# Kernel optimization log

Measured on AMD Instinct MI355X. Metric: run time of the kernel, lower is better.

Reference implementation:

```python
import jax, jax.numpy as jnp
import numpy as np

B, L, C, H, V = 64, 512, 256, 4, 32000
D = C // H
DIL = (1, 2, 4)
WIN = 3
NC = (50, 20)
NEG = -1e9


def setup_inputs() -> dict:
    key = jax.random.key(0)
    ks = jax.random.split(key, 20)
    g = lambda i, shape: jax.random.normal(ks[i], shape, jnp.float32) * 0.05
    Lay = len(DIL)
    x = jax.random.randint(ks[0], (B, L), 0, V)
    emb = g(1, (V, C)).at[0].set(0.0)  # padding_idx=0 row is zero
    return dict(
        x=x, emb=emb, pos=g(2, (L, C)),
        gp_W=g(3, (Lay, C, C)), gp_as=g(4, (Lay, H, D)), gp_ad=g(5, (Lay, H, D)),
        gf_W=g(6, (Lay, C, C)), gf_as=g(7, (Lay, H, D)), gf_ad=g(8, (Lay, H, D)),
        msg_W=g(9, (Lay, C, 2 * C)), msg_b=jnp.zeros((Lay, C), jnp.float32),
        gru_Wih=g(10, (Lay, 3 * C, C)), gru_bih=jnp.zeros((Lay, 3 * C), jnp.float32),
        gru_Whh=g(11, (Lay, 3 * C, C)), gru_bhh=jnp.zeros((Lay, 3 * C), jnp.float32),
        ln_g=jnp.ones((Lay, C), jnp.float32), ln_b=jnp.zeros((Lay, C), jnp.float32),
        pool_w=g(12, (C,)), pool_b=jnp.zeros((), jnp.float32),
        h0_W=g(13, (NC[0], C)), h0_b=jnp.zeros((NC[0],), jnp.float32),
        h1_W=g(14, (NC[1], C)), h1_b=jnp.zeros((NC[1],), jnp.float32),
    )


def _dense_gat(x, W, a_src, a_dst, adj):
    # x: [B,L,C], W: [C_out,C_in], a_*: [H,D], adj: [B,L,L] bool
    b, l, _ = x.shape
    h = jnp.einsum('blc,oc->blo', x, W).reshape(b, l, H, D).transpose(0, 2, 1, 3)  # [B,H,L,D]
    s = jnp.einsum('bhld,hd->bhl', h, a_src)
    d = jnp.einsum('bhld,hd->bhl', h, a_dst)
    e = s[:, :, :, None] + d[:, :, None, :]            # [B,H,L,L]
    e = jnp.where(e > 0, e, 0.2 * e)                   # LeakyReLU(0.2)
    e = jnp.where(adj[:, None, :, :], e, NEG)
    alpha = jax.nn.softmax(e, axis=-1)                 # dropout is identity in eval
    out = jnp.einsum('bhij,bhjd->bhid', alpha, h)
    return out.transpose(0, 2, 1, 3).reshape(b, l, C)


def _forward(x, emb, pos, gp_W, gp_as, gp_ad, gf_W, gf_as, gf_ad,
             msg_W, msg_b, gru_Wih, gru_bih, gru_Whh, gru_bhh,
             ln_g, ln_b, pool_w, pool_b, h0_W, h0_b, h1_W, h1_b):
    mask = x != 0                                      # [B,L]
    mf = mask.astype(jnp.float32)[..., None]           # [B,L,1]
    h = (emb[x] + pos[None, :, :] * mf) * mf
    logical = jnp.clip(jnp.cumsum(mask.astype(jnp.int32), axis=1) - 1, 0)
    valid = mask[:, None, :] & mask[:, :, None]        # [B,L,L]
    eye = jnp.eye(L, dtype=bool)[None]
    for l in range(len(DIL)):
        dil = DIL[l]
        diff = logical[:, :, None] - logical[:, None, :]
        ad = jnp.abs(diff)
        in_win = (ad <= WIN * dil) & (ad % dil == 0)
        adj_p = (valid & in_win & (diff < 0)) | eye
        adj_f = (valid & in_win & (diff > 0)) | eye
        m_p = _dense_gat(h, gp_W[l], gp_as[l], gp_ad[l], adj_p)
        m_f = _dense_gat(h, gf_W[l], gf_as[l], gf_ad[l], adj_f)
        m = jnp.concatenate([m_p, m_f], axis=-1)
        m = jax.nn.relu(jnp.einsum('blk,ck->blc', m, msg_W[l]) + msg_b[l])
        # GRUCell(input=m, hidden=h), PyTorch gate order: r,z,n
        gi = jnp.einsum('blc,gc->blg', m, gru_Wih[l]) + gru_bih[l]
        gh = jnp.einsum('blc,gc->blg', h, gru_Whh[l]) + gru_bhh[l]
        ir, iz, inn = jnp.split(gi, 3, axis=-1)
        hr, hz, hn = jnp.split(gh, 3, axis=-1)
        r = jax.nn.sigmoid(ir + hr)
        z = jax.nn.sigmoid(iz + hz)
        n = jnp.tanh(inn + r * hn)
        h_new = (1.0 - z) * n + z * h
        mu = jnp.mean(h_new, axis=-1, keepdims=True)
        var = jnp.mean(jnp.square(h_new - mu), axis=-1, keepdims=True)
        h_new = (h_new - mu) * jax.lax.rsqrt(var + 1e-5) * ln_g[l] + ln_b[l]
        h = h_new * mf
    # attention pooling over sequence (masked softmax on linear scores)
    sc = jnp.einsum('blc,c->bl', h, pool_w) + pool_b
    sc = jnp.where(mask, sc, NEG)
    a = jax.nn.softmax(sc, axis=-1)
    pooled = jnp.einsum('bl,blc->bc', a, h)            # dropout identity in eval
    o0 = pooled @ h0_W.T + h0_b
    o1 = pooled @ h1_W.T + h1_b
    return jnp.concatenate([o0, o1], axis=-1)          # [B, 50+20]


def reference(x, emb, pos, gp_W, gp_as, gp_ad, gf_W, gf_as, gf_ad,
              msg_W, msg_b, gru_Wih, gru_bih, gru_Whh, gru_bhh,
              ln_g, ln_b, pool_w, pool_b, h0_W, h0_b, h1_W, h1_b):
    return _forward(x, emb, pos, gp_W, gp_as, gp_ad, gf_W, gf_as, gf_ad,
                    msg_W, msg_b, gru_Wih, gru_bih, gru_Whh, gru_bhh,
                    ln_g, ln_b, pool_w, pool_b, h0_W, h0_b, h1_W, h1_b)
```

## Files before the change

### kernel.cpp

```cpp
#include <hip/hip_runtime.h>
#include <math.h>

#define B_ 64
#define L_ 512
#define C_ 256
#define H_ 4
#define LAY 3
#define NEGV -1e9f

#define GF_BIAS  1
#define GF_RELU  2
#define GF_OBF16 4

typedef __attribute__((ext_vector_type(8))) short short8;
typedef __attribute__((ext_vector_type(4))) short short4v;
typedef __attribute__((ext_vector_type(4))) float floatx4;

static __device__ __forceinline__ float rcp_(float x) { return __builtin_amdgcn_rcpf(x); }
static __device__ __forceinline__ float sig_(float x) { return rcp_(1.f + __expf(-x)); }
static __device__ __forceinline__ float tanh_(float x) {
    float e = __expf(2.f * x);
    return 1.f - 2.f * rcp_(e + 1.f);
}

static __device__ __forceinline__ short f2bf(float f) {
    unsigned x = __float_as_uint(f);
    x += 0x7fffu + ((x >> 16) & 1u);
    return (short)(x >> 16);
}
static __device__ __forceinline__ float bf2f(short s) {
    return __uint_as_float(((unsigned)(unsigned short)s) << 16);
}

static __device__ __forceinline__ int tok_swizzle(int blk) {
    int c8 = blk & 7, i = blk >> 3;
    return (c8 + 8 * (i >> 5)) * 128 + (i & 31) * 4;
}

static __device__ __forceinline__ void gl_lds16(const short* g, short* l) {
    __builtin_amdgcn_global_load_lds(
        (const __attribute__((address_space(1))) unsigned int*)g,
        (__attribute__((address_space(3))) unsigned int*)l, 16, 0, 0);
}

#define CF() asm volatile("" ::: "memory")

__global__ void scan_kernel(const int* __restrict__ x, int* __restrict__ mask,
                            int* __restrict__ logical, int* __restrict__ pol,
                            int* __restrict__ nvalid) {
    int b = blockIdx.x, t = threadIdx.x;
    __shared__ int s[L_];
    int m = (x[b * L_ + t] != 0) ? 1 : 0;
    s[t] = m;
    __syncthreads();
    for (int off = 1; off < L_; off <<= 1) {
        int v = (t >= off) ? s[t - off] : 0;
        __syncthreads();
        s[t] += v;
        __syncthreads();
    }
    int cum = s[t];
    int lg = cum - 1; if (lg < 0) lg = 0;
    mask[b * L_ + t] = m;
    logical[b * L_ + t] = lg;
    if (m) pol[b * L_ + lg] = t;
    if (t == L_ - 1) nvalid[b] = cum;
}

__global__ void embed_kernel(const int* __restrict__ x, const float* __restrict__ emb,
                             const float* __restrict__ pos, short* __restrict__ hb) {
    int t = threadIdx.x;
    int bl = tok_swizzle(blockIdx.x) + (t >> 6);
    int lane = t & 63;
    int xv = x[bl];
    float mf = (xv != 0) ? 1.f : 0.f;
    int l = bl & (L_ - 1);
    float4 e = *(const float4*)&emb[(size_t)xv * C_ + lane * 4];
    float4 p = *(const float4*)&pos[(size_t)l * C_ + lane * 4];
    short4v hv4;
    hv4.x = f2bf((e.x + p.x * mf) * mf);
    hv4.y = f2bf((e.y + p.y * mf) * mf);
    hv4.z = f2bf((e.z + p.z * mf) * mf);
    hv4.w = f2bf((e.w + p.w * mf) * mf);
    *(short4v*)&hb[(size_t)bl * C_ + lane * 4] = hv4;
}

__global__ void f2bf_kernel(const float* __restrict__ s, short* __restrict__ d, int n) {
    int i = blockIdx.x * 256 + threadIdx.x;
    if (i < n) d[i] = f2bf(s[i]);
}

__global__ void prep_wcomb(const float* __restrict__ gpW, const float* __restrict__ gfW,
                           const float* __restrict__ gpas, const float* __restrict__ gpad,
                           const float* __restrict__ gfas, const float* __restrict__ gfad,
                           short* __restrict__ Wc) {
    int i = blockIdx.x * 256 + threadIdx.x;
    if (i >= 3 * 640 * 256) return;
    int k = i & 255;
    int r = (i >> 8) % 640;
    int l = i / (640 * 256);
    float v = 0.f;
    if (r < 256) {
        v = gpW[((size_t)l * 256 + r) * 256 + k];
    } else if (r < 512) {
        v = gfW[((size_t)l * 256 + (r - 256)) * 256 + k];
    } else {
        int n = r - 512;
        if (n < 16) {
            int type = n >> 3, dir = (n >> 2) & 1, hh = n & 3;
            const float* a = type ? (dir ? gfad : gpad) : (dir ? gfas : gpas);
            const float* W = dir ? gfW : gpW;
            for (int j = 0; j < 64; j++) {
                float av = a[l * 256 + hh * 64 + j];
                float wv = W[((size_t)l * 256 + hh * 64 + j) * 256 + k];
                v = fmaf(av, wv, v);
            }
        }
    }
    Wc[i] = f2bf(v);
}

__global__ void prep_gru_i(const float* __restrict__ Wih, const float* __restrict__ Whh,
                           short* __restrict__ Bc) {
    int i = blockIdx.x * 256 + threadIdx.x;
    if (i >= 3 * 1024 * 512) return;
    int k = i & 511, np = (i >> 9) & 1023, l = i >> 19;
    int ch = np >> 2, g = np & 3;
    float v = 0.f;
    if (g < 2) {
        v = (k < 256) ? Wih[((size_t)l * 768 + g * 256 + ch) * 256 + k]
                      : Whh[((size_t)l * 768 + g * 256 + ch) * 256 + (k - 256)];
    } else if (g == 2) {
        if (k < 256) v = Wih[((size_t)l * 768 + 512 + ch) * 256 + k];
    } else {
        if (k >= 256) v = Whh[((size_t)l * 768 + 512 + ch) * 256 + (k - 256)];
    }
    Bc[i] = f2bf(v);
}

__global__ void prep_bias4(const float* __restrict__ bih, const float* __restrict__ bhh,
                           float* __restrict__ bc) {
    int i = blockIdx.x * 256 + threadIdx.x;
    if (i >= 3 * 1024) return;
    int np = i & 1023, l = i >> 10;
    int ch = np >> 2, g = np & 3;
    float v;
    if (g < 2)       v = bih[l * 768 + g * 256 + ch] + bhh[l * 768 + g * 256 + ch];
    else if (g == 2) v = bih[l * 768 + 512 + ch];
    else             v = bhh[l * 768 + 512 + ch];
    bc[i] = v;
}

__global__ __launch_bounds__(256) void bgemm(const short* __restrict__ A0,
                                             const short* __restrict__ Bw,
                                             void* __restrict__ Cout,
                                             const float* __restrict__ bias,
                                             int K, int lda, int ldc, int nstore,
                                             int cbBits, int flags) {
    __shared__ short As[128 * 32];
    __shared__ short Bs[128 * 32];
    const int id = blockIdx.x;
    const int nrb8 = gridDim.x >> (3 + cbBits);
    const int j = id >> 3;
    const int cb = j / nrb8;
    const int rb = (id & 7) * nrb8 + (j % nrb8);
    const int tid = threadIdx.x;
    const int wave = tid >> 6, lane = tid & 63;
    const int wm = wave >> 1, wn = wave & 1;
    const size_t arow0 = (size_t)rb * 128;
    const short* Bb = Bw + (size_t)cb * 128 * K;
    floatx4 acc[4][4];
#pragma unroll
    for (int i = 0; i < 4; i++)
#pragma unroll
        for (int jj = 0; jj < 4; jj++) acc[i][jj] = (floatx4)0.f;

    const int srow = lane >> 2;
    const int sq = (lane & 3) * 8;
    const int q = lane >> 4, t16 = lane & 15;

    for (int k0 = 0; k0 < K; k0 += 32) {
        const short* Abase = A0 + arow0 * (size_t)lda + k0;
#pragma unroll
        for (int t = 0; t < 2; ++t) {
            int r = (wave * 2 + t) * 16 + srow;
            gl_lds16(Abase + (size_t)r * lda + sq, &As[r * 32 + sq]);
            gl_lds16(Bb + (size_t)r * K + k0 + sq, &Bs[r * 32 + sq]);
        }
        __syncthreads();
        short8 af[4], bfr[4];
#pragma unroll
        for (int mf = 0; mf < 4; mf++)
            af[mf] = *(const short8*)&As[(wm * 64 + mf * 16 + t16) * 32 + q * 8];
#pragma unroll
        for (int nf = 0; nf < 4; nf++)
            bfr[nf] = *(const short8*)&Bs[(wn * 64 + nf * 16 + t16) * 32 + q * 8];
#pragma unroll
        for (int mf = 0; mf < 4; mf++)
#pragma unroll
            for (int nf = 0; nf < 4; nf++)
                acc[nf][mf] = __builtin_amdgcn_mfma_f32_16x16x32_bf16(
                    bfr[nf], af[mf], acc[nf][mf], 0, 0, 0);
        __syncthreads();
    }

    const int rowbase = rb * 128 + wm * 64;
    const int colbase = cb * 128 + wn * 64;
#pragma unroll
    for (int nf = 0; nf < 4; nf++) {
        int col0 = colbase + nf * 16 + q * 4;
        if (col0 >= nstore) continue;
        float4 bv4 = make_float4(0.f, 0.f, 0.f, 0.f);
        if (flags & GF_BIAS) bv4 = *(const float4*)&bias[col0];
#pragma unroll
        for (int mf = 0; mf < 4; mf++) {
            int row = rowbase + mf * 16 + t16;
            float v0 = acc[nf][mf][0] + bv4.x;
            float v1 = acc[nf][mf][1] + bv4.y;
            float v2 = acc[nf][mf][2] + bv4.z;
            float v3 = acc[nf][mf][3] + bv4.w;
            if (flags & GF_RELU) {
                v0 = fmaxf(v0, 0.f); v1 = fmaxf(v1, 0.f);
                v2 = fmaxf(v2, 0.f); v3 = fmaxf(v3, 0.f);
            }
            size_t base = (size_t)row * ldc + col0;
            if (flags & GF_OBF16) {
                short4v pk;
                pk.x = f2bf(v0); pk.y = f2bf(v1); pk.z = f2bf(v2); pk.w = f2bf(v3);
                *(short4v*)&((short*)Cout)[base] = pk;
            } else {
                float4 pk = make_float4(v0, v1, v2, v3);
                *(float4*)&((float*)Cout)[base] = pk;
            }
        }
    }
}

__global__ __launch_bounds__(256) void projssd_bgemm(const short* __restrict__ A0,
                                                     const short* __restrict__ Bw,
                                                     short* __restrict__ hpb2,
                                                     float* __restrict__ Ssd) {
    __shared__ short As[128 * 32];
    __shared__ short Bs[128 * 32];
    const int id = blockIdx.x;
    const int j = id >> 3;
    const int cb = j >> 5;
    const int rb = ((id & 7) << 5) + (j & 31);
    const int tid = threadIdx.x;
    const int wave = tid >> 6, lane = tid & 63;
    const int wm = wave >> 1, wn = wave & 1;
    const size_t arow0 = (size_t)rb * 128;
    const short* Bb = Bw + (size_t)cb * 128 * 256;
    floatx4 acc[4][4];
#pragma unroll
    for (int i = 0; i < 4; i++)
#pragma unroll
        for (int jj = 0; jj < 4; jj++) acc[i][jj] = (floatx4)0.f;

    const int srow = lane >> 2;
    const int sq = (lane & 3) * 8;
    const int q = lane >> 4, t16 = lane & 15;

    for (int k0 = 0; k0 < 256; k0 += 32) {
        const short* Abase = A0 + arow0 * 256 + k0;
#pragma unroll
        for (int t = 0; t < 2; ++t) {
            int r = (wave * 2 + t) * 16 + srow;
            gl_lds16(Abase + (size_t)r * 256 + sq, &As[r * 32 + sq]);
            gl_lds16(Bb + (size_t)r * 256 + k0 + sq, &Bs[r * 32 + sq]);
        }
        __syncthreads();
        short8 af[4], bfr[4];
#pragma unroll
        for (int mf = 0; mf < 4; mf++)
            af[mf] = *(const short8*)&As[(wm * 64 + mf * 16 + t16) * 32 + q * 8];
#pragma unroll
        for (int nf = 0; nf < 4; nf++)
            bfr[nf] = *(const short8*)&Bs[(wn * 64 + nf * 16 + t16) * 32 + q * 8];
#pragma unroll
        for (int mf = 0; mf < 4; mf++)
#pragma unroll
            for (int nf = 0; nf < 4; nf++)
                acc[nf][mf] = __builtin_amdgcn_mfma_f32_16x16x32_bf16(
                    bfr[nf], af[mf], acc[nf][mf], 0, 0, 0);
        __syncthreads();
    }

    const int rowbase = rb * 128 + wm * 64;
    if (cb < 4) {
        const int colbase = cb * 128 + wn * 64;
#pragma unroll
        for (int nf = 0; nf < 4; nf++) {
            int col0 = colbase + nf * 16 + q * 4;
#pragma unroll
            for (int mf = 0; mf < 4; mf++) {
                int row = rowbase + mf * 16 + t16;
                short4v pk;
                pk.x = f2bf(acc[nf][mf][0]);
                pk.y = f2bf(acc[nf][mf][1]);
                pk.z = f2bf(acc[nf][mf][2]);
                pk.w = f2bf(acc[nf][mf][3]);
                *(short4v*)&hpb2[(size_t)row * 512 + col0] = pk;
            }
        }
    } else {
        if (wn == 0) {
            int col0 = q * 4;
            if (col0 < 16) {
#pragma unroll
                for (int mf = 0; mf < 4; mf++) {
                    int row = rowbase + mf * 16 + t16;
                    float4 pk = make_float4(acc[0][mf][0], acc[0][mf][1],
                                            acc[0][mf][2], acc[0][mf][3]);
                    *(float4*)&Ssd[(size_t)row * 16 + col0] = pk;
                }
            }
        }
    }
}

static __device__ __forceinline__ short8 lds_rd8(const short* p) {
    return *(const short8*)p;
}

template <int MH>
static __device__ __forceinline__ void ld_af(const short* bufA, int wm, int q, int t16,
                                             short8 af[4][2]) {
#pragma unroll
    for (int mfl = 0; mfl < 4; ++mfl) {
        int row = wm * 128 + (MH * 4 + mfl) * 16 + t16;
#pragma unroll
        for (int ks = 0; ks < 2; ++ks) {
            int cg = (ks * 4 + q) ^ (row & 7);
            af[mfl][ks] = lds_rd8(&bufA[row * 64 + cg * 8]);
        }
    }
}

template <int NH>
static __device__ __forceinline__ void ld_bf(const short* bufB, int wn, int q, int t16,
                                             short8 bf[2][2]) {
#pragma unroll
    for (int nfl = 0; nfl < 2; ++nfl) {
        int row = wn * 64 + (NH * 2 + nfl) * 16 + t16;
#pragma unroll
        for (int ks = 0; ks < 2; ++ks) {
            int cg = (ks * 4 + q) ^ (row & 7);
            bf[nfl][ks] = lds_rd8(&bufB[row * 64 + cg * 8]);
        }
    }
}

template <int MH, int NH>
static __device__ __forceinline__ void mfma_q(const short8 af[4][2], const short8 bf[2][2],
                                              floatx4 acc[4][8]) {
    __builtin_amdgcn_s_setprio(1);
#pragma unroll
    for (int ks = 0; ks < 2; ++ks)
#pragma unroll
        for (int mfl = 0; mfl < 4; ++mfl)
#pragma unroll
            for (int nfl = 0; nfl < 2; ++nfl)
                acc[NH * 2 + nfl][MH * 4 + mfl] = __builtin_amdgcn_mfma_f32_16x16x32_bf16(
                    bf[nfl][ks], af[mfl][ks], acc[NH * 2 + nfl][MH * 4 + mfl], 0, 0, 0);
    __builtin_amdgcn_s_setprio(0);
}

__global__ __launch_bounds__(512, 2) void gru_bgemm(const short* __restrict__ mmb,
                                                    const short* __restrict__ hb_in,
                                                    const short* __restrict__ Bw,
                                                    short* __restrict__ hn2b,
                                                    const float* __restrict__ bias4) {
    __shared__ short lds[2][32768];
    const int id = blockIdx.x;
    const int rb = 16 * (id & 7) + (id >> 5);
    const int cb = (id >> 3) & 3;
    const int tid = threadIdx.x;
    const int wave = tid >> 6, lane = tid & 63;
    const int wm = wave >> 2, wn = wave & 3;
    const int q = lane >> 4, t16 = lane & 15;
    const size_t arow0 = (size_t)rb * 256;
    const short* Bb = Bw + (size_t)cb * 256 * 512;
    const int ord0 = (5 + cb) & 7;

    floatx4 acc[4][8];
#pragma unroll
    for (int i = 0; i < 4; i++)
#pragma unroll
        for (int jj = 0; jj < 8; jj++) acc[i][jj] = (floatx4)0.f;

    auto stageA = [&](int i, int Hh) {
        int tt = (ord0 + i) & 7;
        const short* Asrc = (tt < 4) ? (mmb + tt * 64) : (hb_in + (tt - 4) * 64);
        short* bufA = lds[i & 1];
#pragma unroll
        for (int u = 0; u < 2; ++u) {
            int unit = u * 512 + tid;
            int row = Hh * 128 + (unit >> 3);
            int cs = (unit & 7) ^ (row & 7);
            gl_lds16(Asrc + (arow0 + (size_t)row) * 256 + cs * 8,
                     bufA + Hh * 8192 + unit * 8);
        }
    };
    auto stageB = [&](int i, int Hh) {
        int tt = (ord0 + i) & 7;
        short* bufB = lds[i & 1] + 16384;
#pragma unroll
        for (int u = 0; u < 2; ++u) {
            int unit = u * 512 + tid;
            int row = Hh * 128 + (unit >> 3);
            int cs = (unit & 7) ^ (row & 7);
            gl_lds16(Bb + (size_t)row * 512 + tt * 64 + cs * 8,
                     bufB + Hh * 8192 + unit * 8);
        }
    };

    stageA(0, 0); stageA(0, 1); stageB(0, 0); stageB(0, 1);
    stageA(1, 0); stageA(1, 1); stageB(1, 0); stageB(1, 1);
    asm volatile("s_waitcnt vmcnt(8)" ::: "memory");
    CF(); __builtin_amdgcn_s_barrier(); CF();

    short8 af[4][2], b0[2][2], b1[2][2];

#pragma unroll
    for (int t = 0; t < 8; ++t) {
        const short* bufA = lds[t & 1];
        const short* bufB = lds[t & 1] + 16384;

        ld_af<0>(bufA, wm, q, t16, af);
        ld_bf<0>(bufB, wn, q, t16, b0);
        CF(); __builtin_amdgcn_s_barrier();
        asm volatile("s_waitcnt lgkmcnt(0)" ::: "memory");
        __builtin_amdgcn_sched_barrier(0);
        mfma_q<0, 0>(af, b0, acc);
        CF(); __builtin_amdgcn_s_barrier(); CF();

        ld_bf<1>(bufB, wn, q, t16, b1);
        CF(); __builtin_amdgcn_s_barrier();
        asm volatile("s_waitcnt lgkmcnt(0)" ::: "memory");
        __builtin_amdgcn_sched_barrier(0);
        mfma_q<0, 1>(af, b1, acc);
        CF(); __builtin_amdgcn_s_barrier(); CF();

        ld_af<1>(bufA, wm, q, t16, af);
        if (t < 6) { stageB(t + 2, 0); stageB(t + 2, 1); }
        CF(); __builtin_amdgcn_s_barrier();
        asm volatile("s_waitcnt lgkmcnt(0)" ::: "memory");
        __builtin_amdgcn_sched_barrier(0);
        mfma_q<1, 1>(af, b1, acc);
        CF(); __builtin_amdgcn_s_barrier(); CF();

        if (t < 6) { stageA(t + 2, 0); stageA(t + 2, 1); }
        CF(); __builtin_amdgcn_s_barrier();
        mfma_q<1, 0>(af, b0, acc);
        if (t < 6)       asm volatile("s_waitcnt vmcnt(8)" ::: "memory");
        else if (t == 6) asm volatile("s_waitcnt vmcnt(0)" ::: "memory");
        CF(); __builtin_amdgcn_s_barrier(); CF();
    }

    const short* hpt = lds[1];
    short* sO = (short*)lds;
#pragma unroll
    for (int nf = 0; nf < 4; nf++) {
        int chl = wn * 16 + nf * 4 + q;
        int col0 = cb * 256 + wn * 64 + nf * 16 + q * 4;
        float4 bv4 = *(const float4*)&bias4[col0];
#pragma unroll
        for (int mf = 0; mf < 8; mf++) {
            int rowl = wm * 128 + mf * 16 + t16;
            float hp = bf2f(hpt[rowl * 64 + (((chl >> 3) ^ (rowl & 7)) << 3) + (chl & 7)]);
            float r = sig_(acc[nf][mf][0] + bv4.x);
            float z = sig_(acc[nf][mf][1] + bv4.y);
            float nv = tanh_((acc[nf][mf][2] + bv4.z) + r * (acc[nf][mf][3] + bv4.w));
            sO[rowl * 72 + chl] = f2bf((1.f - z) * nv + z * hp);
        }
    }
    __syncthreads();
#pragma unroll
    for (int it = 0; it < 4; ++it) {
        int unit = it * 512 + tid;
        int rowl = unit >> 3, ck = unit & 7;
        *(short8*)&hn2b[(arow0 + rowl) * 256 + cb * 64 + ck * 8] =
            *(const short8*)&sO[rowl * 72 + ck * 8];
    }
}

__global__ __launch_bounds__(256) void ln_kernel(
    const short* __restrict__ hn2b, short* __restrict__ hb,
    const int* __restrict__ mask,
    const float* __restrict__ lng, const float* __restrict__ lnb) {
    int t = threadIdx.x;
    int bl = tok_swizzle(blockIdx.x) + (t >> 6);
    int lane = t & 63;
    short4v v4 = *(const short4v*)&hn2b[(size_t)bl * C_ + lane * 4];
    float v[4] = {bf2f(v4.x), bf2f(v4.y), bf2f(v4.z), bf2f(v4.w)};
    float s = (v[0] + v[1]) + (v[2] + v[3]);
    float ss = (v[0] * v[0] + v[1] * v[1]) + (v[2] * v[2] + v[3] * v[3]);
#pragma unroll
    for (int off = 32; off; off >>= 1) {
        s += __shfl_xor(s, off);
        ss += __shfl_xor(ss, off);
    }
    float mu = s * (1.f / 256.f);
    float var = ss * (1.f / 256.f) - mu * mu;
    float rstd = rsqrtf(fmaxf(var, 0.f) + 1e-5f);
    float4 lg = *(const float4*)&lng[lane * 4];
    float4 lb = *(const float4*)&lnb[lane * 4];
    float mfv = mask[bl] ? 1.f : 0.f;
    short4v yb;
    yb.x = f2bf(((v[0] - mu) * rstd * lg.x + lb.x) * mfv);
    yb.y = f2bf(((v[1] - mu) * rstd * lg.y + lb.y) * mfv);
    yb.z = f2bf(((v[2] - mu) * rstd * lg.z + lb.z) * mfv);
    yb.w = f2bf(((v[3] - mu) * rstd * lg.w + lb.w) * mfv);
    *(short4v*)&hb[(size_t)bl * C_ + lane * 4] = yb;
}

__global__ __launch_bounds__(256) void agg_fused(
    const short* __restrict__ hpb2, const float* __restrict__ S,
    const int* __restrict__ mask, const int* __restrict__ logical,
    const int* __restrict__ pol, const int* __restrict__ nvalid,
    short* __restrict__ m, int dil) {
    int t = threadIdx.x;
    int bl = tok_swizzle(blockIdx.x) + (t >> 6);
    int sub = t & 63;
    int dir = sub >> 5;
    int slot = sub & 31;
    int cb = slot * 8;
    int head = slot >> 3;
    int b = bl >> 9;

    int mi = mask[bl];
    int li = logical[bl];
    int nv = nvalid[b];
    int js[3]; int nn = 0;
    if (mi) {
#pragma unroll
        for (int k = 1; k <= 3; k++) {
            int lj = dir ? (li - k * dil) : (li + k * dil);
            if (lj >= 0 && lj < nv) js[nn++] = pol[b * L_ + lj];
        }
    }
    int sn = dir * 4 + head, dn = 8 + sn;
    float si = S[(size_t)bl * 16 + sn];
    float di = S[(size_t)bl * 16 + dn];
    float e0 = si + di; e0 = e0 > 0.f ? e0 : 0.2f * e0;
    float emax = e0, ev[3];
    for (int k = 0; k < nn; k++) {
        float djv = S[((size_t)(b * L_ + js[k])) * 16 + dn];
        float e = si + djv; e = e > 0.f ? e : 0.2f * e;
        ev[k] = e; emax = fmaxf(emax, e);
    }
    float w0 = __expf(e0 - emax), den = w0;
    float wv[3];
    for (int k = 0; k < nn; k++) { wv[k] = __expf(ev[k] - emax); den += wv[k]; }
    float rden = rcp_(den);

    size_t base = (size_t)bl * 512 + dir * 256 + cb;
    short8 vself = *(const short8*)&hpb2[base];
    float o[8];
#pragma unroll
    for (int j = 0; j < 8; j++) o[j] = w0 * bf2f(vself[j]);
    for (int k = 0; k < nn; k++) {
        short8 vn = *(const short8*)&hpb2[((size_t)(b * L_ + js[k])) * 512 + dir * 256 + cb];
#pragma unroll
        for (int j = 0; j < 8; j++) o[j] = fmaf(wv[k], bf2f(vn[j]), o[j]);
    }
    short8 ov;
#pragma unroll
    for (int j = 0; j < 8; j++) ov[j] = f2bf(o[j] * rden);
    *(short8*)&m[base] = ov;
}

__global__ __launch_bounds__(1024) void pool_head_kernel(
    const short* __restrict__ hb, const int* __restrict__ mask,
    const float* __restrict__ pw, const float* __restrict__ pb,
    const float* __restrict__ h0W, const float* __restrict__ h0b,
    const float* __restrict__ h1W, const float* __restrict__ h1b,
    float* __restrict__ out) {
    int b = blockIdx.x;
    int t = threadIdx.x;
    int lane = t & 63, wave = t >> 6;
    __shared__ float sc[L_];
    __shared__ float red[20];
    __shared__ float part[4][C_];
    __shared__ float pooled[C_];

    float4 wv = *(const float4*)&pw[lane * 4];
    for (int l = wave; l < L_; l += 16) {
        short4v hv = *(const short4v*)&hb[((size_t)b * L_ + l) * C_ + lane * 4];
        float p = bf2f(hv.x) * wv.x + bf2f(hv.y) * wv.y
                + bf2f(hv.z) * wv.z + bf2f(hv.w) * wv.w;
#pragma unroll
        for (int off = 32; off; off >>= 1) p += __shfl_down(p, off);
        if (lane == 0) sc[l] = mask[b * L_ + l] ? (p + pb[0]) : NEGV;
    }
    __syncthreads();

    float v = (t < L_) ? sc[t] : NEGV;
    float mx = v;
#pragma unroll
    for (int off = 32; off; off >>= 1) mx = fmaxf(mx, __shfl_down(mx, off));
    if (lane == 0) red[wave] = mx;
    __syncthreads();
    if (t == 0) {
        float g = red[0];
        for (int i = 1; i < 16; i++) g = fmaxf(g, red[i]);
        red[16] = g;
    }
    __syncthreads();
    float gmax = red[16];
    float e = (t < L_) ? __expf(v - gmax) : 0.f;
    float ssum = e;
#pragma unroll
    for (int off = 32; off; off >>= 1) ssum += __shfl_down(ssum, off);
    if (lane == 0) red[wave] = ssum;
    __syncthreads();
    if (t == 0) {
        float g = 0.f;
        for (int i = 0; i < 16; i++) g += red[i];
        red[17] = 1.f / g;
    }
    __syncthreads();
    if (t < L_) sc[t] = e * red[17];
    __syncthreads();

    int g = t >> 8, c = t & 255;
    const short* hrow = &hb[((size_t)b * L_ + g * 128) * C_ + c];
    const float* scg = &sc[g * 128];
    float a0 = 0.f, a1 = 0.f, a2 = 0.f, a3 = 0.f;
    for (int l = 0; l < 128; l += 4) {
        a0 = fmaf(scg[l + 0], bf2f(hrow[(size_t)(l + 0) * C_]), a0);
        a1 = fmaf(scg[l + 1], bf2f(hrow[(size_t)(l + 1) * C_]), a1);
        a2 = fmaf(scg[l + 2], bf2f(hrow[(size_t)(l + 2) * C_]), a2);
        a3 = fmaf(scg[l + 3], bf2f(hrow[(size_t)(l + 3) * C_]), a3);
    }
    part[g][c] = (a0 + a1) + (a2 + a3);
    __syncthreads();
    if (t < C_) pooled[t] = (part[0][t] + part[1][t]) + (part[2][t] + part[3][t]);
    __syncthreads();

    for (int o = wave; o < 70; o += 16) {
        const float* W = (o < 50) ? (h0W + (size_t)o * C_) : (h1W + (size_t)(o - 50) * C_);
        float bb = (o < 50) ? h0b[o] : h1b[o - 50];
        float4 w4 = *(const float4*)&W[lane * 4];
        float4 p4 = *(const float4*)&pooled[lane * 4];
        float s = p4.x * w4.x + p4.y * w4.y + p4.z * w4.z + p4.w * w4.w;
#pragma unroll
        for (int off = 32; off; off >>= 1) s += __shfl_down(s, off);
        if (lane == 0) out[b * 70 + o] = s + bb;
    }
}

extern "C" void kernel_launch(void* const* d_in, const int* in_sizes, int n_in,
                              void* d_out, int out_size, void* d_ws, size_t ws_size,
                              hipStream_t stream) {
    const int*   x    = (const int*)d_in[0];
    const float* emb  = (const float*)d_in[1];
    const float* pos  = (const float*)d_in[2];
    const float* gpW  = (const float*)d_in[3];
    const float* gpas = (const float*)d_in[4];
    const float* gpad = (const float*)d_in[5];
    const float* gfW  = (const float*)d_in[6];
    const float* gfas = (const float*)d_in[7];
    const float* gfad = (const float*)d_in[8];
    const float* msgW = (const float*)d_in[9];
    const float* msgb = (const float*)d_in[10];
    const float* Wih  = (const float*)d_in[11];
    const float* bih  = (const float*)d_in[12];
    const float* Whh  = (const float*)d_in[13];
    const float* bhh  = (const float*)d_in[14];
    const float* lng  = (const float*)d_in[15];
    const float* lnb  = (const float*)d_in[16];
    const float* pw   = (const float*)d_in[17];
    const float* pb   = (const float*)d_in[18];
    const float* h0W  = (const float*)d_in[19];
    const float* h0b  = (const float*)d_in[20];
    const float* h1W  = (const float*)d_in[21];
    const float* h1b  = (const float*)d_in[22];
    float* out = (float*)d_out;

    const size_t MW = 1024 * 1024;
    float* ws = (float*)d_ws;
    short* hn2b = (short*)ws;
    short* hb   = (short*)(ws + 8 * MW);
    short* mmb  = (short*)(ws + 12 * MW);
    float* Ssd  = ws + 12 * MW;
    short* hpb2 = (short*)(ws + 16 * MW);
    short* mb   = (short*)(ws + 24 * MW);
    short* Wcomb = (short*)(ws + 32 * MW);
    short* msgWb = Wcomb + 3 * 640 * 256;
    short* Bcat  = msgWb + 3 * 256 * 512;
    float* bias4 = (float*)(Bcat + 3 * 1024 * 512);
    int* mask    = (int*)(bias4 + 3 * 1024);
    int* logical = mask + B_ * L_;
    int* pol     = logical + B_ * L_;
    int* nvalid  = pol + B_ * L_;

    prep_wcomb<<<(3 * 640 * 256 + 255) / 256, 256, 0, stream>>>(gpW, gfW, gpas, gpad,
                                                                gfas, gfad, Wcomb);
    f2bf_kernel<<<(3 * 256 * 512 + 255) / 256, 256, 0, stream>>>(msgW, msgWb, 3 * 256 * 512);
    prep_gru_i<<<(3 * 1024 * 512 + 255) / 256, 256, 0, stream>>>(Wih, Whh, Bcat);
    prep_bias4<<<12, 256, 0, stream>>>(bih, bhh, bias4);

    scan_kernel<<<B_, L_, 0, stream>>>(x, mask, logical, pol, nvalid);
    embed_kernel<<<B_ * L_ / 4, 256, 0, stream>>>(x, emb, pos, hb);

    const int DILS[LAY] = {1, 2, 4};

    for (int l = 0; l < LAY; l++) {
        int dil = DILS[l];
        projssd_bgemm<<<256 * 5, 256, 0, stream>>>(hb, Wcomb + (size_t)l * 640 * 256,
                                                   hpb2, Ssd);
        agg_fused<<<8192, 256, 0, stream>>>(hpb2, Ssd, mask, logical, pol, nvalid, mb, dil);
        bgemm<<<256 * 2, 256, 0, stream>>>(mb, msgWb + (size_t)l * 256 * 512,
                                           mmb, msgb + l * C_, 512, 512, 256, 256, 1,
                                           GF_BIAS | GF_RELU | GF_OBF16);
        gru_bgemm<<<512, 512, 0, stream>>>(mmb, hb, Bcat + (size_t)l * 1024 * 512,
                                           hn2b, bias4 + l * 1024);
        ln_kernel<<<8192, 256, 0, stream>>>(hn2b, hb, mask, lng + l * C_, lnb + l * C_);
    }

    pool_head_kernel<<<B_, 1024, 0, stream>>>(hb, mask, pw, pb, h0W, h0b, h1W, h1b, out);
}
```

Measured before the change: 513.4 us.

## Replace generic message GEMM with pipelined 256x128-tile kernel; relax GRU scheduling

The generic 128x128 bgemm used for the message projection is replaced with a dedicated msg_bgemm. It uses 256x128 tiles, 512 threads and double-buffered swizzled LDS staging with async global-to-LDS loads that overlap the MFMA work. The epilogue applies bias and ReLU, converts to bf16, and writes coalesced output through LDS. Separately, the GRU GEMM loop drops its sched_barriers and goes from full unrolling to unroll 2, which gives the compiler more scheduling freedom but may change instruction interleaving.

```diff
diff --git a/kernel.cpp b/kernel.cpp
--- a/kernel.cpp
+++ b/kernel.cpp
@@ -7,10 +7,6 @@
 #define H_ 4
 #define LAY 3
 #define NEGV -1e9f
-
-#define GF_BIAS  1
-#define GF_RELU  2
-#define GF_OBF16 4
 
 typedef __attribute__((ext_vector_type(8))) short short8;
 typedef __attribute__((ext_vector_type(4))) short short4v;
@@ -151,91 +147,6 @@
     bc[i] = v;
 }
 
-__global__ __launch_bounds__(256) void bgemm(const short* __restrict__ A0,
-                                             const short* __restrict__ Bw,
-                                             void* __restrict__ Cout,
-                                             const float* __restrict__ bias,
-                                             int K, int lda, int ldc, int nstore,
-                                             int cbBits, int flags) {
-    __shared__ short As[128 * 32];
-    __shared__ short Bs[128 * 32];
-    const int id = blockIdx.x;
-    const int nrb8 = gridDim.x >> (3 + cbBits);
-    const int j = id >> 3;
-    const int cb = j / nrb8;
-    const int rb = (id & 7) * nrb8 + (j % nrb8);
-    const int tid = threadIdx.x;
-    const int wave = tid >> 6, lane = tid & 63;
-    const int wm = wave >> 1, wn = wave & 1;
-    const size_t arow0 = (size_t)rb * 128;
-    const short* Bb = Bw + (size_t)cb * 128 * K;
-    floatx4 acc[4][4];
-#pragma unroll
-    for (int i = 0; i < 4; i++)
-#pragma unroll
-        for (int jj = 0; jj < 4; jj++) acc[i][jj] = (floatx4)0.f;
-
-    const int srow = lane >> 2;
-    const int sq = (lane & 3) * 8;
-    const int q = lane >> 4, t16 = lane & 15;
-
-    for (int k0 = 0; k0 < K; k0 += 32) {
-        const short* Abase = A0 + arow0 * (size_t)lda + k0;
-#pragma unroll
-        for (int t = 0; t < 2; ++t) {
-            int r = (wave * 2 + t) * 16 + srow;
-            gl_lds16(Abase + (size_t)r * lda + sq, &As[r * 32 + sq]);
-            gl_lds16(Bb + (size_t)r * K + k0 + sq, &Bs[r * 32 + sq]);
-        }
-        __syncthreads();
-        short8 af[4], bfr[4];
-#pragma unroll
-        for (int mf = 0; mf < 4; mf++)
-            af[mf] = *(const short8*)&As[(wm * 64 + mf * 16 + t16) * 32 + q * 8];
-#pragma unroll
-        for (int nf = 0; nf < 4; nf++)
-            bfr[nf] = *(const short8*)&Bs[(wn * 64 + nf * 16 + t16) * 32 + q * 8];
-#pragma unroll
-        for (int mf = 0; mf < 4; mf++)
-#pragma unroll
-            for (int nf = 0; nf < 4; nf++)
-                acc[nf][mf] = __builtin_amdgcn_mfma_f32_16x16x32_bf16(
-                    bfr[nf], af[mf], acc[nf][mf], 0, 0, 0);
-        __syncthreads();
-    }
-
-    const int rowbase = rb * 128 + wm * 64;
-    const int colbase = cb * 128 + wn * 64;
-#pragma unroll
-    for (int nf = 0; nf < 4; nf++) {
-        int col0 = colbase + nf * 16 + q * 4;
-        if (col0 >= nstore) continue;
-        float4 bv4 = make_float4(0.f, 0.f, 0.f, 0.f);
-        if (flags & GF_BIAS) bv4 = *(const float4*)&bias[col0];
-#pragma unroll
-        for (int mf = 0; mf < 4; mf++) {
-            int row = rowbase + mf * 16 + t16;
-            float v0 = acc[nf][mf][0] + bv4.x;
-            float v1 = acc[nf][mf][1] + bv4.y;
-            float v2 = acc[nf][mf][2] + bv4.z;
-            float v3 = acc[nf][mf][3] + bv4.w;
-            if (flags & GF_RELU) {
-                v0 = fmaxf(v0, 0.f); v1 = fmaxf(v1, 0.f);
-                v2 = fmaxf(v2, 0.f); v3 = fmaxf(v3, 0.f);
-            }
-            size_t base = (size_t)row * ldc + col0;
-            if (flags & GF_OBF16) {
-                short4v pk;
-                pk.x = f2bf(v0); pk.y = f2bf(v1); pk.z = f2bf(v2); pk.w = f2bf(v3);
-                *(short4v*)&((short*)Cout)[base] = pk;
-            } else {
-                float4 pk = make_float4(v0, v1, v2, v3);
-                *(float4*)&((float*)Cout)[base] = pk;
-            }
-        }
-    }
-}
-
 __global__ __launch_bounds__(256) void projssd_bgemm(const short* __restrict__ A0,
                                                      const short* __restrict__ Bw,
                                                      short* __restrict__ hpb2,
@@ -351,6 +262,19 @@
     }
 }
 
+static __device__ __forceinline__ void ld_bf32(const short* bufB, int wn, int q, int t16,
+                                               short8 bf[2][2]) {
+#pragma unroll
+    for (int nfl = 0; nfl < 2; ++nfl) {
+        int row = wn * 32 + nfl * 16 + t16;
+#pragma unroll
+        for (int ks = 0; ks < 2; ++ks) {
+            int cg = (ks * 4 + q) ^ (row & 7);
+            bf[nfl][ks] = lds_rd8(&bufB[row * 64 + cg * 8]);
+        }
+    }
+}
+
 template <int MH, int NH>
 static __device__ __forceinline__ void mfma_q(const short8 af[4][2], const short8 bf[2][2],
                                               floatx4 acc[4][8]) {
@@ -363,6 +287,21 @@
             for (int nfl = 0; nfl < 2; ++nfl)
                 acc[NH * 2 + nfl][MH * 4 + mfl] = __builtin_amdgcn_mfma_f32_16x16x32_bf16(
                     bf[nfl][ks], af[mfl][ks], acc[NH * 2 + nfl][MH * 4 + mfl], 0, 0, 0);
+    __builtin_amdgcn_s_setprio(0);
+}
+
+template <int MH>
+static __device__ __forceinline__ void mfma_m(const short8 af[4][2], const short8 bf[2][2],
+                                              floatx4 acc[2][8]) {
+    __builtin_amdgcn_s_setprio(1);
+#pragma unroll
+    for (int ks = 0; ks < 2; ++ks)
+#pragma unroll
+        for (int mfl = 0; mfl < 4; ++mfl)
+#pragma unroll
+            for (int nfl = 0; nfl < 2; ++nfl)
+                acc[nfl][MH * 4 + mfl] = __builtin_amdgcn_mfma_f32_16x16x32_bf16(
+                    bf[nfl][ks], af[mfl][ks], acc[nfl][MH * 4 + mfl], 0, 0, 0);
     __builtin_amdgcn_s_setprio(0);
 }
 
@@ -422,7 +361,7 @@
 
     short8 af[4][2], b0[2][2], b1[2][2];
 
-#pragma unroll
+#pragma unroll 2
     for (int t = 0; t < 8; ++t) {
         const short* bufA = lds[t & 1];
         const short* bufB = lds[t & 1] + 16384;
@@ -431,14 +370,12 @@
         ld_bf<0>(bufB, wn, q, t16, b0);
         CF(); __builtin_amdgcn_s_barrier();
         asm volatile("s_waitcnt lgkmcnt(0)" ::: "memory");
-        __builtin_amdgcn_sched_barrier(0);
         mfma_q<0, 0>(af, b0, acc);
         CF(); __builtin_amdgcn_s_barrier(); CF();
 
         ld_bf<1>(bufB, wn, q, t16, b1);
         CF(); __builtin_amdgcn_s_barrier();
         asm volatile("s_waitcnt lgkmcnt(0)" ::: "memory");
-        __builtin_amdgcn_sched_barrier(0);
         mfma_q<0, 1>(af, b1, acc);
         CF(); __builtin_amdgcn_s_barrier(); CF();
 
@@ -446,7 +383,6 @@
         if (t < 6) { stageB(t + 2, 0); stageB(t + 2, 1); }
         CF(); __builtin_amdgcn_s_barrier();
         asm volatile("s_waitcnt lgkmcnt(0)" ::: "memory");
-        __builtin_amdgcn_sched_barrier(0);
         mfma_q<1, 1>(af, b1, acc);
         CF(); __builtin_amdgcn_s_barrier(); CF();
 
@@ -482,6 +418,106 @@
         int rowl = unit >> 3, ck = unit & 7;
         *(short8*)&hn2b[(arow0 + rowl) * 256 + cb * 64 + ck * 8] =
             *(const short8*)&sO[rowl * 72 + ck * 8];
+    }
+}
+
+__global__ __launch_bounds__(512, 2) void msg_bgemm(const short* __restrict__ A0,
+                                                    const short* __restrict__ Bw,
+                                                    short* __restrict__ Cout,
+                                                    const float* __restrict__ bias) {
+    __shared__ short lds[2][24576];
+    const int id = blockIdx.x;
+    const int j = id >> 3;
+    const int rb = (id & 7) * 16 + (j & 15);
+    const int cb = j >> 4;
+    const int tid = threadIdx.x;
+    const int wave = tid >> 6, lane = tid & 63;
+    const int wm = wave >> 2, wn = wave & 3;
+    const int q = lane >> 4, t16 = lane & 15;
+    const size_t arow0 = (size_t)rb * 256;
+    const short* Bb = Bw + (size_t)cb * 128 * 512;
+
+    floatx4 acc[2][8];
+#pragma unroll
+    for (int i = 0; i < 2; i++)
+#pragma unroll
+        for (int jj = 0; jj < 8; jj++) acc[i][jj] = (floatx4)0.f;
+
+    auto stageA = [&](int t, int Hh) {
+        short* bufA = lds[t & 1];
+#pragma unroll
+        for (int u = 0; u < 2; ++u) {
+            int unit = u * 512 + tid;
+            int row = Hh * 128 + (unit >> 3);
+            int cs = (unit & 7) ^ (row & 7);
+            gl_lds16(A0 + (arow0 + (size_t)row) * 512 + t * 64 + cs * 8,
+                     bufA + Hh * 8192 + unit * 8);
+        }
+    };
+    auto stageB = [&](int t) {
+        short* bufB = lds[t & 1] + 16384;
+#pragma unroll
+        for (int u = 0; u < 2; ++u) {
+            int unit = u * 512 + tid;
+            int row = unit >> 3;
+            int cs = (unit & 7) ^ (row & 7);
+            gl_lds16(Bb + (size_t)row * 512 + t * 64 + cs * 8, bufB + unit * 8);
+        }
+    };
+
+    stageA(0, 0); stageA(0, 1); stageB(0); stageB(1);
+    asm volatile("s_waitcnt vmcnt(2)" ::: "memory");
+    CF(); __builtin_amdgcn_s_barrier(); CF();
+
+    short8 af[4][2], bfr[2][2];
+
+#pragma unroll 2
+    for (int t = 0; t < 8; ++t) {
+        const short* bufA = lds[t & 1];
+        const short* bufB = lds[t & 1] + 16384;
+
+        ld_af<0>(bufA, wm, q, t16, af);
+        ld_bf32(bufB, wn, q, t16, bfr);
+        if (t < 7) { stageA(t + 1, 0); stageA(t + 1, 1); }
+        CF(); __builtin_amdgcn_s_barrier();
+        asm volatile("s_waitcnt lgkmcnt(0)" ::: "memory");
+        mfma_m<0>(af, bfr, acc);
+        CF(); __builtin_amdgcn_s_barrier(); CF();
+
+        ld_af<1>(bufA, wm, q, t16, af);
+        if (t < 6) stageB(t + 2);
+        CF(); __builtin_amdgcn_s_barrier();
+        asm volatile("s_waitcnt lgkmcnt(0)" ::: "memory");
+        mfma_m<1>(af, bfr, acc);
+        if (t < 6)       asm volatile("s_waitcnt vmcnt(2)" ::: "memory");
+        else if (t == 6) asm volatile("s_waitcnt vmcnt(0)" ::: "memory");
+        CF(); __builtin_amdgcn_s_barrier(); CF();
+    }
+
+    short* sO = (short*)lds;
+#pragma unroll
+    for (int nf = 0; nf < 2; nf++) {
+        int chl = wn * 32 + nf * 16 + q * 4;
+        int col0 = cb * 128 + chl;
+        float4 bv4 = *(const float4*)&bias[col0];
+#pragma unroll
+        for (int mf = 0; mf < 8; mf++) {
+            int rowl = wm * 128 + mf * 16 + t16;
+            short4v pk;
+            pk.x = f2bf(fmaxf(acc[nf][mf][0] + bv4.x, 0.f));
+            pk.y = f2bf(fmaxf(acc[nf][mf][1] + bv4.y, 0.f));
+            pk.z = f2bf(fmaxf(acc[nf][mf][2] + bv4.z, 0.f));
+            pk.w = f2bf(fmaxf(acc[nf][mf][3] + bv4.w, 0.f));
+            *(short4v*)&sO[rowl * 132 + chl] = pk;
+        }
+    }
+    __syncthreads();
+#pragma unroll
+    for (int it = 0; it < 8; ++it) {
+        int unit = it * 512 + tid;
+        int rowl = unit >> 4, ck = unit & 15;
+        *(short8*)&Cout[(arow0 + rowl) * 256 + cb * 128 + ck * 8] =
+            *(const short8*)&sO[rowl * 132 + ck * 8];
     }
 }
 
@@ -712,9 +748,8 @@
         projssd_bgemm<<<256 * 5, 256, 0, stream>>>(hb, Wcomb + (size_t)l * 640 * 256,
                                                    hpb2, Ssd);
         agg_fused<<<8192, 256, 0, stream>>>(hpb2, Ssd, mask, logical, pol, nvalid, mb, dil);
-        bgemm<<<256 * 2, 256, 0, stream>>>(mb, msgWb + (size_t)l * 256 * 512,
-                                           mmb, msgb + l * C_, 512, 512, 256, 256, 1,
-                                           GF_BIAS | GF_RELU | GF_OBF16);
+        msg_bgemm<<<256, 512, 0, stream>>>(mb, msgWb + (size_t)l * 256 * 512,
+                                           mmb, msgb + l * C_);
         gru_bgemm<<<512, 512, 0, stream>>>(mmb, hb, Bcat + (size_t)l * 1024 * 512,
                                            hn2b, bias4 + l * 1024);
         ln_kernel<<<8192, 256, 0, stream>>>(hn2b, hb, mask, lng + l * C_, lnb + l * C_);
```

Result: faster. 500.5 us (-2.5%).
